# Performance work log

Hardware: AMD Instinct MI355X
Metric: run time of the kernel (lower is better)

## Reference

```python
import jax, jax.numpy as jnp
import numpy as np

C_IN, C_OUT, K, H, W = 16, 16, 3, 1024, 1024
PAD = 1  # 'same' padding for 3x3 stride-1


def setup_inputs() -> dict:
    key = jax.random.key(0)
    kx, kw, kb = jax.random.split(key, 3)
    x = jax.random.normal(kx, (1, C_IN, H, W), dtype=jnp.float32)
    weight = jax.random.normal(kw, (C_OUT, C_IN, K, K), dtype=jnp.float32) * 0.05
    bias = jax.random.normal(kb, (C_OUT,), dtype=jnp.float32) * 0.05
    return {"x": x, "weight": weight, "bias": bias}


def reference(x, weight, bias):
    # Original module: im2col (unfold) + matmul + reshape + bias add.
    # Mathematically identical to a dense 2D convolution (cross-correlation),
    # expressed here as the fused implicit-GEMM conv primitive.
    out = jax.lax.conv_general_dilated(
        x, weight,
        window_strides=(1, 1),
        padding=((PAD, PAD), (PAD, PAD)),
        dimension_numbers=("NCHW", "OIHW", "NCHW"),
    )  # [1, C_OUT, H, W]
    # out_unf.view(*output_shape) drops the batch dim (batch must be 1)
    return out[0] + bias[:, None, None]
```

## Files before the change

### kernel.cpp

```cpp
#include <hip/hip_runtime.h>


#define HH 1024
#define WW 1024
#define CIN 16
#define COUT 16
#define TW 64
#define TH 16
#define LROWS (TH + 2)
#define LCOLS (TW + 2)
#define PIX 16

typedef short v8s __attribute__((ext_vector_type(8)));
typedef float v4f __attribute__((ext_vector_type(4)));

__device__ __forceinline__ unsigned short f32_bf16(float f) {
    union { float f; unsigned int u; } v;
    v.f = f;
    unsigned int u = v.u;
    u += 0x7fffu + ((u >> 16) & 1u);
    return (unsigned short)(u >> 16);
}

__global__ __launch_bounds__(256, 4)
void conv3x3_mfma(const float* __restrict__ x,
                  const float* __restrict__ wgt,
                  const float* __restrict__ bias,
                  float* __restrict__ out) {
    __shared__ __align__(16) unsigned short sm[LROWS * LCOLS * PIX];

    const int tid = threadIdx.x;
    const int h0 = blockIdx.y * TH;
    const int w0 = blockIdx.x * TW;

    const int E = LROWS * LCOLS * CIN;
    for (int e = tid; e < E; e += 256) {
        int c = e % LCOLS;
        int t = e / LCOLS;
        int r = t % LROWS;
        int cin = t / LROWS;
        int gh = h0 - 1 + r;
        int gw = w0 - 1 + c;
        float v = 0.0f;
        if ((unsigned)gh < (unsigned)HH && (unsigned)gw < (unsigned)WW)
            v = x[cin * (HH * WW) + gh * WW + gw];
        sm[(r * LCOLS + c) * PIX + cin] = f32_bf16(v);
    }

    const int lane = tid & 63;
    const int wave = tid >> 6;
    const int m = lane & 15;
    const int q = lane >> 4;
    const int qh = q >> 1;
    const int qc = (q & 1) * 8;

    v8s a1[3], a2[3];
    for (int kw = 0; kw < 3; ++kw) {
        for (int j = 0; j < 8; ++j) {
            a1[kw][j] = (short)f32_bf16(wgt[((m * CIN + (qc + j)) * 3 + qh) * 3 + kw]);
            short t2 = 0;
            if (q < 2)
                t2 = (short)f32_bf16(wgt[((m * CIN + (q * 8 + j)) * 3 + 2) * 3 + kw]);
            a2[kw][j] = t2;
        }
    }
    float bl[4];
    #pragma unroll
    for (int i = 0; i < 4; ++i) bl[i] = bias[q * 4 + i];

    __syncthreads();

    const int colbase = wave * 16 + m;
    for (int r = 0; r < TH; ++r) {
        v4f accA = {0.f, 0.f, 0.f, 0.f};
        v4f accB = {0.f, 0.f, 0.f, 0.f};
        #pragma unroll
        for (int kw = 0; kw < 3; ++kw) {
            const int col = colbase + kw;
            v8s b1 = *(const v8s*)&sm[((r + qh) * LCOLS + col) * PIX + qc];
            accA = __builtin_amdgcn_mfma_f32_16x16x32_bf16(a1[kw], b1, accA, 0, 0, 0);
            v8s b2 = {0, 0, 0, 0, 0, 0, 0, 0};
            if (q < 2)
                b2 = *(const v8s*)&sm[((r + 2) * LCOLS + col) * PIX + q * 8];
            accB = __builtin_amdgcn_mfma_f32_16x16x32_bf16(a2[kw], b2, accB, 0, 0, 0);
        }
        const int h = h0 + r;
        float* op = out + h * WW + (w0 + colbase);
        #pragma unroll
        for (int i = 0; i < 4; ++i) {
            op[(q * 4 + i) * (HH * WW)] = accA[i] + accB[i] + bl[i];
        }
    }
}

extern "C" void kernel_launch(void* const* d_in, const int* in_sizes, int n_in,
                              void* d_out, int out_size, void* d_ws, size_t ws_size,
                              hipStream_t stream) {
    const float* x = (const float*)d_in[0];
    const float* w = (const float*)d_in[1];
    const float* b = (const float*)d_in[2];
    float* out = (float*)d_out;
    dim3 grid(WW / TW, HH / TH);
    conv3x3_mfma<<<grid, dim3(256), 0, stream>>>(x, w, b, out);
}
```

Before: 148.0 us.

## Pre-pack input into padded bf16 NHWC workspace and load tiles via global_load_lds

Adds a packing kernel that converts the fp32 NCHW input into a zero-padded bf16 channels-last buffer in the workspace. The conv kernel then fills its shared-memory tile with direct 16-byte global-to-LDS loads, with no per-element conversion, bounds checks or scattered stores. The aim is to remove the uncoalesced, transposing halo load. The cost is an extra kernel launch and an extra round trip of the input through memory. The old kernel is kept as a fallback for when the workspace is too small.

```diff
diff --git a/kernel.cpp b/kernel.cpp
--- a/kernel.cpp
+++ b/kernel.cpp
@@ -10,29 +10,144 @@
 #define LROWS (TH + 2)
 #define LCOLS (TW + 2)
 #define PIX 16
+#define XPW 1026
 
 typedef short v8s __attribute__((ext_vector_type(8)));
 typedef float v4f __attribute__((ext_vector_type(4)));
+typedef unsigned int u32;
 
 __device__ __forceinline__ unsigned short f32_bf16(float f) {
-    union { float f; unsigned int u; } v;
+    union { float f; u32 u; } v;
     v.f = f;
-    unsigned int u = v.u;
+    u32 u = v.u;
     u += 0x7fffu + ((u >> 16) & 1u);
     return (unsigned short)(u >> 16);
 }
 
+__global__ __launch_bounds__(256)
+void conv_pack(const float* __restrict__ x, unsigned short* __restrict__ xp) {
+    const int hp = blockIdx.x;
+    const int h = hp - 1;
+    if ((unsigned)h >= (unsigned)HH) {
+        uint4 z = {0u, 0u, 0u, 0u};
+        uint4* dst = (uint4*)(xp + (size_t)hp * XPW * PIX);
+        for (int i = threadIdx.x; i < XPW * 2; i += 256) dst[i] = z;
+        return;
+    }
+    if (threadIdx.x < 4) {
+        uint4 z = {0u, 0u, 0u, 0u};
+        if (threadIdx.x < 2) {
+            uint4* d0 = (uint4*)(xp + (size_t)hp * XPW * PIX);
+            d0[threadIdx.x] = z;
+        } else {
+            uint4* d1 = (uint4*)(xp + ((size_t)hp * XPW + 1025) * PIX);
+            d1[threadIdx.x - 2] = z;
+        }
+    }
+    const int t = threadIdx.x;
+    for (int wbase = 0; wbase < WW; wbase += 512) {
+        const int w = wbase + 2 * t;
+        const float* src = x + (size_t)h * WW + w;
+        u32 p0[8], p1[8];
+        #pragma unroll
+        for (int c = 0; c < CIN; c += 2) {
+            float2 va = *(const float2*)(src + (size_t)c * HH * WW);
+            float2 vb = *(const float2*)(src + (size_t)(c + 1) * HH * WW);
+            p0[c >> 1] = (u32)f32_bf16(va.x) | ((u32)f32_bf16(vb.x) << 16);
+            p1[c >> 1] = (u32)f32_bf16(va.y) | ((u32)f32_bf16(vb.y) << 16);
+        }
+        uint4* dst = (uint4*)(xp + ((size_t)hp * XPW + (w + 1)) * PIX);
+        dst[0] = *(uint4*)&p0[0];
+        dst[1] = *(uint4*)&p0[4];
+        dst[2] = *(uint4*)&p1[0];
+        dst[3] = *(uint4*)&p1[4];
+    }
+}
+
+
+typedef const __attribute__((address_space(1))) u32* gptr_t;
+typedef __attribute__((address_space(3))) u32* lptr_t;
+
 __global__ __launch_bounds__(256, 4)
-void conv3x3_mfma(const float* __restrict__ x,
+void conv3x3_mfma(const unsigned short* __restrict__ xp,
                   const float* __restrict__ wgt,
                   const float* __restrict__ bias,
                   float* __restrict__ out) {
     __shared__ __align__(16) unsigned short sm[LROWS * LCOLS * PIX];
 
     const int tid = threadIdx.x;
+    const int lane = tid & 63;
+    const int wave = tid >> 6;
     const int h0 = blockIdx.y * TH;
     const int w0 = blockIdx.x * TW;
 
+    const unsigned char* xpb = (const unsigned char*)xp;
+    #pragma unroll
+    for (int it = 0; it < 10; ++it) {
+        int cid = it * 256 + wave * 64 + lane;
+        if (cid < (LROWS * LCOLS * PIX * 2) / 16) {
+            int r = cid / 132;
+            int o = cid - r * 132;
+            const unsigned char* g =
+                xpb + ((size_t)(h0 + r) * XPW + w0) * (PIX * 2) + (size_t)o * 16;
+            lptr_t l = (lptr_t)((__attribute__((address_space(3))) unsigned char*)sm +
+                                (it * 256 + wave * 64) * 16);
+            __builtin_amdgcn_global_load_lds((gptr_t)g, l, 16, 0, 0);
+        }
+    }
+
+    const int m = lane & 15;
+    const int q = lane >> 4;
+    const int qh = q >> 1;
+    const int qc = (q & 1) * 8;
+
+    v8s a1[3], a2[3];
+    for (int kw = 0; kw < 3; ++kw) {
+        for (int j = 0; j < 8; ++j) {
+            a1[kw][j] = (short)f32_bf16(wgt[((m * CIN + (qc + j)) * 3 + qh) * 3 + kw]);
+            short t2 = 0;
+            if (q < 2)
+                t2 = (short)f32_bf16(wgt[((m * CIN + (q * 8 + j)) * 3 + 2) * 3 + kw]);
+            a2[kw][j] = t2;
+        }
+    }
+    float bl[4];
+    #pragma unroll
+    for (int i = 0; i < 4; ++i) bl[i] = bias[q * 4 + i];
+
+    __syncthreads();
+
+    const int colbase = wave * 16 + m;
+    for (int r = 0; r < TH; ++r) {
+        v4f accA = {0.f, 0.f, 0.f, 0.f};
+        v4f accB = {0.f, 0.f, 0.f, 0.f};
+        #pragma unroll
+        for (int kw = 0; kw < 3; ++kw) {
+            const int col = colbase + kw;
+            v8s b1 = *(const v8s*)&sm[((r + qh) * LCOLS + col) * PIX + qc];
+            accA = __builtin_amdgcn_mfma_f32_16x16x32_bf16(a1[kw], b1, accA, 0, 0, 0);
+            v8s b2 = {0, 0, 0, 0, 0, 0, 0, 0};
+            if (q < 2)
+                b2 = *(const v8s*)&sm[((r + 2) * LCOLS + col) * PIX + q * 8];
+            accB = __builtin_amdgcn_mfma_f32_16x16x32_bf16(a2[kw], b2, accB, 0, 0, 0);
+        }
+        const int h = h0 + r;
+        float* op = out + (size_t)h * WW + (w0 + colbase);
+        #pragma unroll
+        for (int i = 0; i < 4; ++i)
+            op[(size_t)(q * 4 + i) * (HH * WW)] = accA[i] + accB[i] + bl[i];
+    }
+}
+
+__global__ __launch_bounds__(256, 4)
+void conv3x3_mfma_fb(const float* __restrict__ x,
+                     const float* __restrict__ wgt,
+                     const float* __restrict__ bias,
+                     float* __restrict__ out) {
+    __shared__ __align__(16) unsigned short sm[LROWS * LCOLS * PIX];
+    const int tid = threadIdx.x;
+    const int h0 = blockIdx.y * TH;
+    const int w0 = blockIdx.x * TW;
     const int E = LROWS * LCOLS * CIN;
     for (int e = tid; e < E; e += 256) {
         int c = e % LCOLS;
@@ -46,14 +161,12 @@
             v = x[cin * (HH * WW) + gh * WW + gw];
         sm[(r * LCOLS + c) * PIX + cin] = f32_bf16(v);
     }
-
     const int lane = tid & 63;
     const int wave = tid >> 6;
     const int m = lane & 15;
     const int q = lane >> 4;
     const int qh = q >> 1;
     const int qc = (q & 1) * 8;
-
     v8s a1[3], a2[3];
     for (int kw = 0; kw < 3; ++kw) {
         for (int j = 0; j < 8; ++j) {
@@ -67,9 +180,7 @@
     float bl[4];
     #pragma unroll
     for (int i = 0; i < 4; ++i) bl[i] = bias[q * 4 + i];
-
     __syncthreads();
-
     const int colbase = wave * 16 + m;
     for (int r = 0; r < TH; ++r) {
         v4f accA = {0.f, 0.f, 0.f, 0.f};
@@ -87,9 +198,8 @@
         const int h = h0 + r;
         float* op = out + h * WW + (w0 + colbase);
         #pragma unroll
-        for (int i = 0; i < 4; ++i) {
+        for (int i = 0; i < 4; ++i)
             op[(q * 4 + i) * (HH * WW)] = accA[i] + accB[i] + bl[i];
-        }
     }
 }
 
@@ -100,6 +210,14 @@
     const float* w = (const float*)d_in[1];
     const float* b = (const float*)d_in[2];
     float* out = (float*)d_out;
-    dim3 grid(WW / TW, HH / TH);
-    conv3x3_mfma<<<grid, dim3(256), 0, stream>>>(x, w, b, out);
-}
+    const size_t need = (size_t)XPW * XPW * PIX * sizeof(unsigned short);
+    if (ws_size >= need) {
+        unsigned short* xp = (unsigned short*)d_ws;
+        conv_pack<<<dim3(XPW), dim3(256), 0, stream>>>(x, xp);
+        dim3 grid(WW / TW, HH / TH);
+        conv3x3_mfma<<<grid, dim3(256), 0, stream>>>(xp, w, b, out);
+    } else {
+        dim3 grid(WW / TW, HH / TH);
+        conv3x3_mfma_fb<<<grid, dim3(256), 0, stream>>>(x, w, b, out);
+    }
+}
```

Result: no change. 149.2 us (+0.9%).

## Pack 3x3 taps into five K=32 MFMAs with swizzled per-pixel LDS staging

Applied to the files above, without the earlier changes.

The 144-long reduction (9 taps by 16 channels) is regrouped into 18 half-channel chunks spread over 5 MFMA k-groups. This replaces the previous 6 MFMAs (two of them half-zero) and their two accumulators with 5 MFMAs on one accumulator. The LDS fill now has each thread load all 16 channels of one pixel and write two packed 16-byte stores, using an XOR swizzle on the two half-slots to reduce bank conflicts, instead of scattering 2-byte stores element by element. The row loop is unrolled by 4. The per-pixel fill issues strided global loads across channel planes, but each load still coalesces across threads along width.

```diff
diff --git a/kernel.cpp b/kernel.cpp
--- a/kernel.cpp
+++ b/kernel.cpp
@@ -10,58 +10,82 @@
 #define LROWS (TH + 2)
 #define LCOLS (TW + 2)
 #define PIX 16
+#define NPIX (LROWS * LCOLS)
 
 typedef short v8s __attribute__((ext_vector_type(8)));
 typedef float v4f __attribute__((ext_vector_type(4)));
+typedef unsigned int u32;
 
 __device__ __forceinline__ unsigned short f32_bf16(float f) {
-    union { float f; unsigned int u; } v;
+    union { float f; u32 u; } v;
     v.f = f;
-    unsigned int u = v.u;
+    u32 u = v.u;
     u += 0x7fffu + ((u >> 16) & 1u);
     return (unsigned short)(u >> 16);
 }
 
 __global__ __launch_bounds__(256, 4)
-void conv3x3_mfma(const float* __restrict__ x,
-                  const float* __restrict__ wgt,
-                  const float* __restrict__ bias,
-                  float* __restrict__ out) {
-    __shared__ __align__(16) unsigned short sm[LROWS * LCOLS * PIX];
+void conv3x3_fused(const float* __restrict__ x,
+                   const float* __restrict__ wgt,
+                   const float* __restrict__ bias,
+                   float* __restrict__ out) {
+    __shared__ __align__(16) unsigned short sm[NPIX * PIX];
 
     const int tid = threadIdx.x;
+    const int lane = tid & 63;
+    const int wave = tid >> 6;
     const int h0 = blockIdx.y * TH;
     const int w0 = blockIdx.x * TW;
 
-    const int E = LROWS * LCOLS * CIN;
-    for (int e = tid; e < E; e += 256) {
-        int c = e % LCOLS;
-        int t = e / LCOLS;
-        int r = t % LROWS;
-        int cin = t / LROWS;
-        int gh = h0 - 1 + r;
-        int gw = w0 - 1 + c;
-        float v = 0.0f;
-        if ((unsigned)gh < (unsigned)HH && (unsigned)gw < (unsigned)WW)
-            v = x[cin * (HH * WW) + gh * WW + gw];
-        sm[(r * LCOLS + c) * PIX + cin] = f32_bf16(v);
+    #pragma unroll
+    for (int i = 0; i < 5; ++i) {
+        const int p = i * 256 + tid;
+        if (p < NPIX) {
+            const int r = p / LCOLS;
+            const int col = p - r * LCOLS;
+            const int gh = h0 - 1 + r;
+            const int gw = w0 - 1 + col;
+            float f[CIN];
+            #pragma unroll
+            for (int c = 0; c < CIN; ++c) f[c] = 0.0f;
+            if ((unsigned)gh < (unsigned)HH && (unsigned)gw < (unsigned)WW) {
+                const float* src = x + (size_t)gh * WW + gw;
+                #pragma unroll
+                for (int c = 0; c < CIN; ++c)
+                    f[c] = src[(size_t)c * (HH * WW)];
+            }
+            u32 pk[8];
+            #pragma unroll
+            for (int c = 0; c < 8; ++c)
+                pk[c] = (u32)f32_bf16(f[2 * c]) | ((u32)f32_bf16(f[2 * c + 1]) << 16);
+            const int c0 = p * 2;
+            const int sel = (c0 >> 3) & 1;
+            uint4* dst = (uint4*)(sm + c0 * 8);
+            dst[sel] = *(uint4*)&pk[0];
+            dst[1 - sel] = *(uint4*)&pk[4];
+        }
     }
 
-    const int lane = tid & 63;
-    const int wave = tid >> 6;
     const int m = lane & 15;
     const int q = lane >> 4;
-    const int qh = q >> 1;
-    const int qc = (q & 1) * 8;
+    const int colbase = wave * 16 + m;
 
-    v8s a1[3], a2[3];
-    for (int kw = 0; kw < 3; ++kw) {
+    v8s a[5];
+    int Kofs[5];
+    #pragma unroll
+    for (int g5 = 0; g5 < 5; ++g5) {
+        int t = 4 * g5 + q;
+        int tt = t > 17 ? 17 : t;
+        int khkw = tt >> 1;
+        int kh = khkw / 3;
+        int kw = khkw - 3 * kh;
+        int half = tt & 1;
+        Kofs[g5] = (kh * LCOLS + colbase + kw) * 2 + half;
+        bool valid = t < 18;
+        #pragma unroll
         for (int j = 0; j < 8; ++j) {
-            a1[kw][j] = (short)f32_bf16(wgt[((m * CIN + (qc + j)) * 3 + qh) * 3 + kw]);
-            short t2 = 0;
-            if (q < 2)
-                t2 = (short)f32_bf16(wgt[((m * CIN + (q * 8 + j)) * 3 + 2) * 3 + kw]);
-            a2[kw][j] = t2;
+            float wv = valid ? wgt[((m * CIN + half * 8 + j) * 3 + kh) * 3 + kw] : 0.0f;
+            a[g5][j] = (short)f32_bf16(wv);
         }
     }
     float bl[4];
@@ -70,26 +94,20 @@
 
     __syncthreads();
 
-    const int colbase = wave * 16 + m;
+    #pragma unroll 4
     for (int r = 0; r < TH; ++r) {
-        v4f accA = {0.f, 0.f, 0.f, 0.f};
-        v4f accB = {0.f, 0.f, 0.f, 0.f};
+        v4f acc = {0.f, 0.f, 0.f, 0.f};
         #pragma unroll
-        for (int kw = 0; kw < 3; ++kw) {
-            const int col = colbase + kw;
-            v8s b1 = *(const v8s*)&sm[((r + qh) * LCOLS + col) * PIX + qc];
-            accA = __builtin_amdgcn_mfma_f32_16x16x32_bf16(a1[kw], b1, accA, 0, 0, 0);
-            v8s b2 = {0, 0, 0, 0, 0, 0, 0, 0};
-            if (q < 2)
-                b2 = *(const v8s*)&sm[((r + 2) * LCOLS + col) * PIX + q * 8];
-            accB = __builtin_amdgcn_mfma_f32_16x16x32_bf16(a2[kw], b2, accB, 0, 0, 0);
+        for (int g5 = 0; g5 < 5; ++g5) {
+            int c = r * (LCOLS * 2) + Kofs[g5];
+            int phys = c ^ ((c >> 3) & 1);
+            v8s b = *(const v8s*)(sm + phys * 8);
+            acc = __builtin_amdgcn_mfma_f32_16x16x32_bf16(a[g5], b, acc, 0, 0, 0);
         }
-        const int h = h0 + r;
-        float* op = out + h * WW + (w0 + colbase);
+        float* op = out + (size_t)(h0 + r) * WW + (w0 + colbase);
         #pragma unroll
-        for (int i = 0; i < 4; ++i) {
-            op[(q * 4 + i) * (HH * WW)] = accA[i] + accB[i] + bl[i];
-        }
+        for (int i = 0; i < 4; ++i)
+            op[(size_t)(q * 4 + i) * (HH * WW)] = acc[i] + bl[i];
     }
 }
 
@@ -101,5 +119,5 @@
     const float* b = (const float*)d_in[2];
     float* out = (float*)d_out;
     dim3 grid(WW / TW, HH / TH);
-    conv3x3_mfma<<<grid, dim3(256), 0, stream>>>(x, w, b, out);
+    conv3x3_fused<<<grid, dim3(256), 0, stream>>>(x, w, b, out);
 }
```

Measured after the change: 140.2 us. 5.2% less time.
